# Optimization experiments

Hardware: AMD Instinct MI355X
Metric: run time of the kernel (lower is better)

The kernel has to match this reference:

```python
import jax, jax.numpy as jnp
import numpy as np

N = 50000
E = 800000
IN_C = 128
HID = 256
OUT_C = 51


def graph_conv(x, edge_index, edge_weight, w_rel, b_rel, w_root):
    # PyG GraphConv: out = lin_rel(aggr_add(w_e * x_src)) + lin_root(x)
    src, dst = edge_index[0], edge_index[1]
    msgs = x[src] * edge_weight[:, None]            # [E, F]
    agg = jax.ops.segment_sum(msgs, dst, num_segments=x.shape[0])  # [N, F]
    return agg @ w_rel + b_rel + x @ w_root


def setup_inputs() -> dict:
    key = jax.random.key(0)
    ks = jax.random.split(key, 10)
    s = lambda fan_in: 1.0 / np.sqrt(fan_in)
    return {
        "x0": jax.random.normal(ks[0], (N, IN_C), jnp.float32),
        "edge_index": jax.random.randint(ks[1], (2, E), 0, N, jnp.int64),
        "edge_weight": jax.random.uniform(ks[2], (E,), jnp.float32),
        "conv1_w_rel": jax.random.uniform(ks[3], (IN_C, HID), jnp.float32, -s(IN_C), s(IN_C)),
        "conv1_b_rel": jnp.zeros((HID,), jnp.float32),
        "conv1_w_root": jax.random.uniform(ks[4], (IN_C, HID), jnp.float32, -s(IN_C), s(IN_C)),
        "conv2_w_rel": jax.random.uniform(ks[5], (HID, HID), jnp.float32, -s(HID), s(HID)),
        "conv2_b_rel": jnp.zeros((HID,), jnp.float32),
        "conv2_w_root": jax.random.uniform(ks[6], (HID, HID), jnp.float32, -s(HID), s(HID)),
        "lin_w": jax.random.uniform(ks[7], (2 * HID, OUT_C), jnp.float32, -s(2 * HID), s(2 * HID)),
        "lin_b": jnp.zeros((OUT_C,), jnp.float32),
    }


def reference(x0, edge_index, edge_weight,
              conv1_w_rel, conv1_b_rel, conv1_w_root,
              conv2_w_rel, conv2_b_rel, conv2_w_root,
              lin_w, lin_b):
    # eval mode: dropout is identity
    x1 = jax.nn.relu(graph_conv(x0, edge_index, edge_weight, conv1_w_rel, conv1_b_rel, conv1_w_root))
    x2 = jax.nn.relu(graph_conv(x1, edge_index, edge_weight, conv2_w_rel, conv2_b_rel, conv2_w_root))
    x = jnp.concatenate([x1, x2], axis=-1)          # [N, 2H]
    return x @ lin_w + lin_b                         # [N, OUT_C]
```

## Files before the change

### kernel.cpp

```cpp
#include <hip/hip_runtime.h>
#include <hip/hip_bf16.h>

#define N_NODES 50000
#define N_EDGES 800000
#define IN_CH   128
#define HID     256
#define OUTC    51

typedef __attribute__((ext_vector_type(8))) short  bf16x8;
typedef __attribute__((ext_vector_type(4))) float  f32x4;
typedef __attribute__((ext_vector_type(2))) float  f32x2;
typedef __attribute__((ext_vector_type(4))) unsigned int u32x4;

__device__ __forceinline__ float bf2f(unsigned short u) {
    union { unsigned int i; float f; } v; v.i = ((unsigned int)u) << 16; return v.f;
}
__device__ __forceinline__ unsigned short f2bf(float f) {
    union { float f; unsigned int i; } v; v.f = f;
    unsigned int u = v.i;
    unsigned int r = (u + 0x7fffu + ((u >> 16) & 1u)) >> 16;
    return (unsigned short)r;
}
__device__ __forceinline__ unsigned short ldbf(const void* p, long i, int isf) {
    return isf ? f2bf(((const float*)p)[i]) : ((const unsigned short*)p)[i];
}
__device__ __forceinline__ float ldf(const void* p, long i, int isf) {
    return isf ? ((const float*)p)[i] : bf2f(((const unsigned short*)p)[i]);
}
__device__ __forceinline__ void load_edge_nt(const int* __restrict__ ei, int e, int is64,
                                             int* src, int* dst) {
    if (is64) { *src = __builtin_nontemporal_load(ei + 2 * e);
                *dst = __builtin_nontemporal_load(ei + 2 * (N_EDGES + e)); }
    else      { *src = __builtin_nontemporal_load(ei + e);
                *dst = __builtin_nontemporal_load(ei + N_EDGES + e); }
}

typedef const __attribute__((address_space(1))) unsigned int* gas_u32;
typedef __attribute__((address_space(3))) unsigned int* las_u32;
__device__ __forceinline__ void cp16(const void* g, void* l) {
    __builtin_amdgcn_global_load_lds((gas_u32)g, (las_u32)l, 16, 0, 0);
}

#define EBLK 1024
#define HB   ((N_EDGES + EBLK - 1) / EBLK)
#define NBKT ((N_NODES + 255) / 256)

__global__ __launch_bounds__(256) void init_kernel(const unsigned int* __restrict__ x0w,
                                                   int* __restrict__ flags,
                                                   const int* __restrict__ ei) {
    int tid = threadIdx.x;
    if (blockIdx.x == 0) {
        if (tid < 64) {
            unsigned int w = x0w[tid];
            unsigned int ex = (w >> 7) & 0xFFu;
            unsigned long long bm = __ballot(ex >= 0x60u && ex <= 0x90u);
            if (tid == 0) flags[0] = (__popcll(bm) >= 48) ? 0 : 1;
        }
        return;
    }
    __shared__ int any;
    if (tid == 0) any = 0;
    __syncthreads();
    int acc = 0;
    for (int s = 0; s < 8; s++) {
        int i = (tid * 8 + s) * (N_EDGES / 2048);
        acc |= ei[2 * i + 1];
    }
    if (acc != 0) any = 1;
    __syncthreads();
    if (tid == 0) flags[1] = any;
}

__global__ void prep_all_kernel(const void* __restrict__ x0, int cb,
                                const void* __restrict__ w1r, const void* __restrict__ w1x,
                                const void* __restrict__ w2r, const void* __restrict__ w2x,
                                const void* __restrict__ lw,
                                const void* __restrict__ b1h, const void* __restrict__ b2h,
                                const void* __restrict__ lbh, const int* __restrict__ flags,
                                unsigned short* __restrict__ x0bf,
                                unsigned short* __restrict__ Bt1, unsigned short* __restrict__ Bt2,
                                unsigned short* __restrict__ Bt3,
                                float* __restrict__ b1, float* __restrict__ b2, float* __restrict__ b3,
                                const int* __restrict__ ei, unsigned int* __restrict__ bc,
                                int pblocks) {
    __shared__ unsigned int cnt[NBKT];
    int isf = flags[0];
    if ((int)blockIdx.x < cb) {
        if (!isf) return;
        long t0 = ((long)blockIdx.x * 256 + threadIdx.x) * 8;
        const float* xf = (const float*)x0;
        f32x4 v0 = *(const f32x4*)(xf + t0);
        f32x4 v1 = *(const f32x4*)(xf + t0 + 4);
        u32x4 pk;
        pk[0] = (unsigned int)f2bf(v0[0]) | ((unsigned int)f2bf(v0[1]) << 16);
        pk[1] = (unsigned int)f2bf(v0[2]) | ((unsigned int)f2bf(v0[3]) << 16);
        pk[2] = (unsigned int)f2bf(v1[0]) | ((unsigned int)f2bf(v1[1]) << 16);
        pk[3] = (unsigned int)f2bf(v1[2]) | ((unsigned int)f2bf(v1[3]) << 16);
        *(u32x4*)(x0bf + t0) = pk;
        return;
    }
    int rb = blockIdx.x - cb;
    if (rb >= pblocks) {
        int b = rb - pblocks;
        int tid = threadIdx.x;
        if (tid < NBKT) cnt[tid] = 0;
        __syncthreads();
        int is64 = (flags[1] == 0);
        int e0 = b * EBLK;
#pragma unroll
        for (int u = 0; u < 4; u++) {
            int e = e0 + u * 256 + tid;
            if (e < N_EDGES) {
                int src, dst; load_edge_nt(ei, e, is64, &src, &dst);
                if ((unsigned)src < N_NODES && (unsigned)dst < N_NODES)
                    atomicAdd(&cnt[dst >> 8], 1u);
            }
        }
        __syncthreads();
        if (tid < NBKT) bc[tid * HB + b] = cnt[tid];
        return;
    }
    int t = rb * 256 + threadIdx.x;
    if (t < 256 * 256) {
        int n = t >> 8, k = t & 255;
        Bt1[n * 256 + k] = (k < 128) ? ldbf(w1r, k * 256 + n, isf) : ldbf(w1x, (k - 128) * 256 + n, isf);
        return;
    }
    t -= 256 * 256;
    if (t < 256 * 512) {
        int n = t >> 9, k = t & 511;
        Bt2[n * 512 + k] = (k < 256) ? ldbf(w2r, k * 256 + n, isf) : ldbf(w2x, (k - 256) * 256 + n, isf);
        return;
    }
    t -= 256 * 512;
    if (t < 64 * 512) {
        int n = t >> 9, k = t & 511;
        Bt3[n * 512 + k] = (n < OUTC) ? ldbf(lw, k * OUTC + n, isf) : (unsigned short)0;
        return;
    }
    t -= 64 * 512;
    if (t < 256) { b1[t] = ldf(b1h, t, isf); return; }
    t -= 256;
    if (t < 256) { b2[t] = ldf(b2h, t, isf); return; }
    t -= 256;
    if (t < 64)  { b3[t] = (t < OUTC) ? ldf(lbh, t, isf) : 0.0f; return; }
}

__global__ __launch_bounds__(1024) void s1_kernel(const unsigned int* __restrict__ bc,
                                                  unsigned int* __restrict__ pbase,
                                                  unsigned int* __restrict__ total) {
    __shared__ unsigned int sd[1024];
    int b = blockIdx.x, tid = threadIdx.x;
    unsigned int v = (tid < HB) ? bc[b * HB + tid] : 0u;
    sd[tid] = v;
    __syncthreads();
    for (int off = 1; off < 1024; off <<= 1) {
        unsigned int t = (tid >= off) ? sd[tid - off] : 0u;
        __syncthreads();
        sd[tid] += t;
        __syncthreads();
    }
    if (tid < HB) pbase[tid * NBKT + b] = sd[tid] - v;
    if (tid == 1023) total[b] = sd[1023];
}

__global__ __launch_bounds__(256) void f1_kernel(const int* __restrict__ ei, const void* __restrict__ ew,
                                                 const int* __restrict__ flags,
                                                 const unsigned int* __restrict__ pbase,
                                                 const unsigned int* __restrict__ btot,
                                                 uint2* __restrict__ rec) {
    __shared__ unsigned int cur[NBKT];
    __shared__ unsigned int sb[256];
    int tid = threadIdx.x;
    unsigned int v = (tid < NBKT) ? btot[tid] : 0u;
    sb[tid] = v;
    __syncthreads();
    for (int off = 1; off < 256; off <<= 1) {
        unsigned int t = (tid >= off) ? sb[tid - off] : 0u;
        __syncthreads();
        sb[tid] += t;
        __syncthreads();
    }
    if (tid < NBKT) cur[tid] = (sb[tid] - v) + pbase[blockIdx.x * NBKT + tid];
    __syncthreads();
    int is64 = (flags[1] == 0);
    int isf = flags[0];
    int e0 = blockIdx.x * EBLK;
#pragma unroll
    for (int u = 0; u < 4; u++) {
        int e = e0 + u * 256 + tid;
        if (e < N_EDGES) {
            int src, dst; load_edge_nt(ei, e, is64, &src, &dst);
            if ((unsigned)src < N_NODES && (unsigned)dst < N_NODES) {
                unsigned int w = ldbf(ew, e, isf);
                unsigned int pos = atomicAdd(&cur[dst >> 8], 1u);
                uint2 r; r.x = (w << 16) | (unsigned)src; r.y = (unsigned)dst;
                rec[pos] = r;
            }
        }
    }
}

__global__ __launch_bounds__(512) void f2_kernel(const uint2* __restrict__ rec,
                                                 const unsigned int* __restrict__ btot,
                                                 int* __restrict__ rp, unsigned int* __restrict__ cw) {
    __shared__ unsigned int sb[256], c2[256], sc[256], cur2[256];
    int tid = threadIdx.x, b = blockIdx.x;
    unsigned int vb = 0;
    if (tid < 256) { vb = (tid < NBKT) ? btot[tid] : 0u; sb[tid] = vb; }
    __syncthreads();
    for (int off = 1; off < 256; off <<= 1) {
        unsigned int t = (tid < 256 && tid >= off) ? sb[tid - off] : 0u;
        __syncthreads();
        if (tid < 256) sb[tid] += t;
        __syncthreads();
    }
    unsigned int s0 = (b > 0) ? sb[b - 1] : 0u;
    unsigned int e0 = sb[b];
    if (b == 0 && tid == 0) rp[N_NODES] = (int)sb[NBKT - 1];
    if (tid < 256) c2[tid] = 0;
    __syncthreads();
    for (unsigned int pos = s0 + tid; pos < e0; pos += 512)
        atomicAdd(&c2[rec[pos].y & 255u], 1u);
    __syncthreads();
    unsigned int v = 0;
    if (tid < 256) { v = c2[tid]; sc[tid] = v; }
    __syncthreads();
    for (int off = 1; off < 256; off <<= 1) {
        unsigned int t = (tid < 256 && tid >= off) ? sc[tid - off] : 0u;
        __syncthreads();
        if (tid < 256) sc[tid] += t;
        __syncthreads();
    }
    if (tid < 256) {
        unsigned int start = s0 + sc[tid] - v;
        int node = b * 256 + tid;
        if (node < N_NODES) rp[node] = (int)start;
        cur2[tid] = start;
    }
    __syncthreads();
    for (unsigned int pos = s0 + tid; pos < e0; pos += 512) {
        uint2 r = rec[pos];
        unsigned int p = atomicAdd(&cur2[r.y & 255u], 1u);
        cw[p] = r.x;
    }
}

__global__ __launch_bounds__(256) void zout_kernel(unsigned short* __restrict__ out, long n) {
    long t = (long)blockIdx.x * 256 + threadIdx.x;
    if (t < n) out[t] = 0;
}

__global__ __launch_bounds__(256) void agg1_kernel(const unsigned short* __restrict__ x0raw,
                                                   const unsigned short* __restrict__ x0conv,
                                                   int use_conv, const int* __restrict__ flags,
                                                   const int* __restrict__ rp, const unsigned int* __restrict__ cw,
                                                   unsigned short* __restrict__ X12) {
    const unsigned short* x0b = (use_conv && flags[0]) ? x0conv : x0raw;
    int r = blockIdx.x * 16 + (threadIdx.x >> 4);
    if (r >= N_NODES) return;
    int l = threadIdx.x & 15;
    int grpbase = threadIdx.x & 48;
    int js = rp[r], je = rp[r + 1];
    if (js < 0) js = 0;
    if (je > N_EDGES) je = N_EDGES;
    float a0 = 0.f, a1 = 0.f, a2 = 0.f, a3 = 0.f;
    float a4 = 0.f, a5 = 0.f, a6 = 0.f, a7 = 0.f;
    for (int base = js; base < je; base += 16) {
        int n = je - base; if (n > 16) n = 16;
        int idx = base + l; if (idx >= je) idx = je - 1;
        unsigned int rec = __builtin_nontemporal_load(cw + idx);
        for (int j = 0; j < n; j += 4) {
            int m = n - j; if (m > 4) m = 4;
            unsigned int vv[4]; u32x4 q[4];
#pragma unroll
            for (int u = 0; u < 4; u++) vv[u] = __shfl(rec, grpbase + j + u);
#pragma unroll
            for (int u = 0; u < 4; u++) if (u < m)
                q[u] = *(const u32x4*)(x0b + (long)(vv[u] & 0xFFFFu) * 128 + l * 8);
#pragma unroll
            for (int u = 0; u < 4; u++) if (u < m) {
                float w = bf2f((unsigned short)(vv[u] >> 16));
                a0 += w * bf2f((unsigned short)(q[u][0] & 0xffffu));
                a1 += w * bf2f((unsigned short)(q[u][0] >> 16));
                a2 += w * bf2f((unsigned short)(q[u][1] & 0xffffu));
                a3 += w * bf2f((unsigned short)(q[u][1] >> 16));
                a4 += w * bf2f((unsigned short)(q[u][2] & 0xffffu));
                a5 += w * bf2f((unsigned short)(q[u][2] >> 16));
                a6 += w * bf2f((unsigned short)(q[u][3] & 0xffffu));
                a7 += w * bf2f((unsigned short)(q[u][3] >> 16));
            }
        }
    }
    u32x4 pk;
    pk[0] = (unsigned int)f2bf(a0) | ((unsigned int)f2bf(a1) << 16);
    pk[1] = (unsigned int)f2bf(a2) | ((unsigned int)f2bf(a3) << 16);
    pk[2] = (unsigned int)f2bf(a4) | ((unsigned int)f2bf(a5) << 16);
    pk[3] = (unsigned int)f2bf(a6) | ((unsigned int)f2bf(a7) << 16);
    *(u32x4*)&X12[(long)r * 512 + 256 + l * 8] = pk;
}

__global__ __launch_bounds__(256) void agg2_kernel(const int* __restrict__ rp, const unsigned int* __restrict__ cw,
                                                   unsigned short* __restrict__ X12,
                                                   const unsigned char* __restrict__ x1f8,
                                                   const int* __restrict__ flags, int f8mode) {
    int usef8 = (f8mode == 2) || (f8mode == 1 && flags[0] == 0);
    int r = blockIdx.x * 16 + (threadIdx.x >> 4);
    if (r >= N_NODES) return;
    int l = threadIdx.x & 15;
    int grpbase = threadIdx.x & 48;
    int js = rp[r], je = rp[r + 1];
    if (js < 0) js = 0;
    if (je > N_EDGES) je = N_EDGES;
    float a[16];
#pragma unroll
    for (int c = 0; c < 16; c++) a[c] = 0.f;
    if (usef8) {
        for (int base = js; base < je; base += 16) {
            int n = je - base; if (n > 16) n = 16;
            int idx = base + l; if (idx >= je) idx = je - 1;
            unsigned int rec = __builtin_nontemporal_load(cw + idx);
            for (int j = 0; j < n; j += 4) {
                int m = n - j; if (m > 4) m = 4;
                unsigned int vv[4]; u32x4 q[4];
#pragma unroll
                for (int u = 0; u < 4; u++) vv[u] = __shfl(rec, grpbase + j + u);
#pragma unroll
                for (int u = 0; u < 4; u++) if (u < m)
                    q[u] = *(const u32x4*)(x1f8 + (long)(vv[u] & 0xFFFFu) * 256 + l * 16);
#pragma unroll
                for (int u = 0; u < 4; u++) if (u < m) {
                    float w = bf2f((unsigned short)(vv[u] >> 16));
#pragma unroll
                    for (int c = 0; c < 4; c++) {
                        f32x2 plo = __builtin_amdgcn_cvt_pk_f32_fp8((int)q[u][c], false);
                        f32x2 phi = __builtin_amdgcn_cvt_pk_f32_fp8((int)q[u][c], true);
                        a[c * 4 + 0] += w * plo.x; a[c * 4 + 1] += w * plo.y;
                        a[c * 4 + 2] += w * phi.x; a[c * 4 + 3] += w * phi.y;
                    }
                }
            }
        }
    } else {
        for (int base = js; base < je; base += 16) {
            int n = je - base; if (n > 16) n = 16;
            int idx = base + l; if (idx >= je) idx = je - 1;
            unsigned int rec = __builtin_nontemporal_load(cw + idx);
            for (int j = 0; j < n; j += 4) {
                int m = n - j; if (m > 4) m = 4;
                unsigned int vv[4]; u32x4 q0[4], q1[4];
#pragma unroll
                for (int u = 0; u < 4; u++) vv[u] = __shfl(rec, grpbase + j + u);
#pragma unroll
                for (int u = 0; u < 4; u++) if (u < m) {
                    const unsigned short* sp = X12 + (long)(vv[u] & 0xFFFFu) * 512 + l * 16;
                    q0[u] = *(const u32x4*)sp;
                    q1[u] = *(const u32x4*)(sp + 8);
                }
#pragma unroll
                for (int u = 0; u < 4; u++) if (u < m) {
                    float w = bf2f((unsigned short)(vv[u] >> 16));
#pragma unroll
                    for (int c = 0; c < 4; c++) {
                        a[c * 2 + 0] += w * bf2f((unsigned short)(q0[u][c] & 0xffffu));
                        a[c * 2 + 1] += w * bf2f((unsigned short)(q0[u][c] >> 16));
                        a[8 + c * 2 + 0] += w * bf2f((unsigned short)(q1[u][c] & 0xffffu));
                        a[8 + c * 2 + 1] += w * bf2f((unsigned short)(q1[u][c] >> 16));
                    }
                }
            }
        }
    }
    u32x4 p0, p1;
#pragma unroll
    for (int c = 0; c < 4; c++) {
        p0[c] = (unsigned int)f2bf(a[c * 2]) | ((unsigned int)f2bf(a[c * 2 + 1]) << 16);
        p1[c] = (unsigned int)f2bf(a[8 + c * 2]) | ((unsigned int)f2bf(a[8 + c * 2 + 1]) << 16);
    }
    unsigned short* op = &X12[(long)r * 512 + 256 + l * 16];
    *(u32x4*)op = p0;
    *(u32x4*)(op + 8) = p1;
}

__global__ __launch_bounds__(512) void gemm_big_kernel(
    const unsigned short* __restrict__ Aagg, int lda_agg, int Kagg,
    const unsigned short* __restrict__ AxRaw, const unsigned short* __restrict__ AxConv,
    int use_conv, int lda_x,
    const unsigned short* __restrict__ Bt, int K,
    const float* __restrict__ bias, const int* __restrict__ flags,
    unsigned short* __restrict__ out, int ldo, int ocol, int M,
    unsigned char* __restrict__ x1f8, int f8mode) {
    __shared__ __align__(16) unsigned short As[128][64];
    __shared__ __align__(16) unsigned short Bs[256][64];
    const unsigned short* Ax = (use_conv && flags[0]) ? AxConv : AxRaw;
    int dof8 = (f8mode == 2) || (f8mode == 1 && flags[0] == 0);
    int tid = threadIdx.x;
    int bm0 = blockIdx.x * 128;
    int wave = tid >> 6, lane = tid & 63;
    int wm = wave >> 2, wn = wave & 3;
    int quad = lane >> 4, l16 = lane & 15;
    int lr = lane >> 3;
    int sc = (lane & 7) ^ lr;

    f32x4 acc[4][4];
#pragma unroll
    for (int mt = 0; mt < 4; mt++)
#pragma unroll
        for (int nt = 0; nt < 4; nt++) acc[mt][nt] = (f32x4){0.f, 0.f, 0.f, 0.f};

    for (int k0 = 0; k0 < K; k0 += 64) {
        const unsigned short* srcp;
        int stride, koff;
        if (k0 < Kagg) { srcp = Aagg; stride = lda_agg; koff = k0; }
        else           { srcp = Ax;   stride = lda_x;   koff = k0 - Kagg; }
#pragma unroll
        for (int i = 0; i < 2; i++) {
            int t = wave * 2 + i;
            int r = t * 8 + lr;
            int gr = bm0 + r; if (gr >= M) gr = M - 1;
            cp16(srcp + (long)gr * stride + koff + sc * 8, (char*)As + t * 1024);
        }
#pragma unroll
        for (int i = 0; i < 4; i++) {
            int t = wave * 4 + i;
            int r = t * 8 + lr;
            cp16(Bt + (long)r * K + k0 + sc * 8, (char*)Bs + t * 1024);
        }
        __syncthreads();
#pragma unroll
        for (int kc = 0; kc < 64; kc += 32) {
            int k8 = (kc >> 3) + quad;
            int swz = (k8 ^ (l16 & 7)) << 4;
            bf16x8 a[4], b[4];
#pragma unroll
            for (int mt = 0; mt < 4; mt++) {
                int row = wm * 64 + mt * 16 + l16;
                a[mt] = *(const bf16x8*)((const char*)As + row * 128 + swz);
            }
#pragma unroll
            for (int nt = 0; nt < 4; nt++) {
                int row = wn * 64 + nt * 16 + l16;
                b[nt] = *(const bf16x8*)((const char*)Bs + row * 128 + swz);
            }
#pragma unroll
            for (int mt = 0; mt < 4; mt++)
#pragma unroll
                for (int nt = 0; nt < 4; nt++)
                    acc[mt][nt] = __builtin_amdgcn_mfma_f32_16x16x32_bf16(a[mt], b[nt], acc[mt][nt], 0, 0, 0);
        }
        __syncthreads();
    }

#pragma unroll
    for (int mt = 0; mt < 4; mt++) {
#pragma unroll
        for (int nt = 0; nt < 4; nt++) {
            f32x4 a = acc[mt][nt];
            int colI = wn * 64 + nt * 16 + l16;
            float bv = bias[colI];
#pragma unroll
            for (int rr = 0; rr < 4; rr++) {
                int row = bm0 + wm * 64 + mt * 16 + quad * 4 + rr;
                if (row < M) {
                    float v = a[rr] + bv;
                    v = v > 0.f ? v : 0.f;
                    out[(long)row * ldo + ocol + colI] = f2bf(v);
                    if (dof8) {
                        int p = __builtin_amdgcn_cvt_pk_fp8_f32(v, v, 0, false);
                        x1f8[(long)row * 256 + colI] = (unsigned char)(p & 0xff);
                    }
                }
            }
        }
    }
}

__global__ __launch_bounds__(256) void gemm_head_kernel(
    const unsigned short* __restrict__ Ax, int lda_x,
    const unsigned short* __restrict__ Bt, int K,
    const float* __restrict__ bias,
    void* __restrict__ out, int ldo,
    int M, int realN, const int* __restrict__ flagF) {
    __shared__ __align__(16) unsigned short As[64][64];
    __shared__ __align__(16) unsigned short Bs[64][64];
    int tid = threadIdx.x;
    int bm0 = blockIdx.x * 64;
    int wave = tid >> 6, lane = tid & 63;
    int wm = wave >> 1, wn = wave & 1;
    int quad = lane >> 4, l16 = lane & 15;
    int lr = lane >> 3;
    int sc = (lane & 7) ^ lr;

    f32x4 acc[2][2];
#pragma unroll
    for (int mt = 0; mt < 2; mt++)
#pragma unroll
        for (int nt = 0; nt < 2; nt++) acc[mt][nt] = (f32x4){0.f, 0.f, 0.f, 0.f};

    for (int k0 = 0; k0 < K; k0 += 64) {
#pragma unroll
        for (int i = 0; i < 2; i++) {
            int t = wave * 2 + i;
            int r = t * 8 + lr;
            int gr = bm0 + r; if (gr >= M) gr = M - 1;
            cp16(Ax + (long)gr * lda_x + k0 + sc * 8, (char*)As + t * 1024);
        }
#pragma unroll
        for (int i = 0; i < 2; i++) {
            int t = wave * 2 + i;
            int r = t * 8 + lr;
            cp16(Bt + (long)r * K + k0 + sc * 8, (char*)Bs + t * 1024);
        }
        __syncthreads();
#pragma unroll
        for (int kc = 0; kc < 64; kc += 32) {
            int k8 = (kc >> 3) + quad;
            int swz = (k8 ^ (l16 & 7)) << 4;
            bf16x8 a0 = *(const bf16x8*)((const char*)As + (wm * 32 + l16) * 128 + swz);
            bf16x8 a1 = *(const bf16x8*)((const char*)As + (wm * 32 + 16 + l16) * 128 + swz);
#pragma unroll
            for (int nt = 0; nt < 2; nt++) {
                bf16x8 b = *(const bf16x8*)((const char*)Bs + (wn * 32 + nt * 16 + l16) * 128 + swz);
                acc[0][nt] = __builtin_amdgcn_mfma_f32_16x16x32_bf16(a0, b, acc[0][nt], 0, 0, 0);
                acc[1][nt] = __builtin_amdgcn_mfma_f32_16x16x32_bf16(a1, b, acc[1][nt], 0, 0, 0);
            }
        }
        __syncthreads();
    }

    int out_f32 = *flagF;
#pragma unroll
    for (int mt = 0; mt < 2; mt++) {
#pragma unroll
        for (int nt = 0; nt < 2; nt++) {
            f32x4 a = acc[mt][nt];
            int colI = wn * 32 + nt * 16 + l16;
            float bv = bias[colI];
#pragma unroll
            for (int rr = 0; rr < 4; rr++) {
                int row = bm0 + wm * 32 + mt * 16 + quad * 4 + rr;
                if (row < M && colI < realN) {
                    float v = a[rr] + bv;
                    long idx = (long)row * ldo + colI;
                    if (out_f32) ((float*)out)[idx] = v;
                    else ((unsigned short*)out)[idx] = f2bf(v);
                }
            }
        }
    }
}

extern "C" void kernel_launch(void* const* d_in, const int* in_sizes, int n_in,
                              void* d_out, int out_size, void* d_ws, size_t ws_size,
                              hipStream_t stream) {
    const void* x0  = d_in[0];
    const int*  ei  = (const int*)d_in[1];
    const void* ew  = d_in[2];
    const void* w1r = d_in[3];
    const void* b1h = d_in[4];
    const void* w1x = d_in[5];
    const void* w2r = d_in[6];
    const void* b2h = d_in[7];
    const void* w2x = d_in[8];
    const void* lw  = d_in[9];
    const void* lbh = d_in[10];

    char* ws = (char*)d_ws;
    unsigned short* X12     = (unsigned short*)(ws);
    unsigned int*   cw      = (unsigned int*)(ws + 51200000);
    int*            row_ptr = (int*)(ws + 54400000);
    unsigned short* Bt1     = (unsigned short*)(ws + 54800128);
    unsigned short* Bt2     = (unsigned short*)(ws + 54931200);
    unsigned short* Bt3     = (unsigned short*)(ws + 55193344);
    float*          b1      = (float*)(ws + 55258880);
    float*          b2      = (float*)(ws + 55259904);
    float*          b3      = (float*)(ws + 55260928);
    int*            flags   = (int*)(ws + 55261184);
    unsigned short* x0bf    = (unsigned short*)(ws + 55262272);
    unsigned char*  x1f8sep = (unsigned char*)(ws + 68062272);
    const size_t NEED_NOCONV = 55262272;
    const size_t NEED_FULL   = 68062272;
    const size_t NEED_F8SEP  = 80862272;

    uint2*        rec   = (uint2*)(ws);
    unsigned int* bc    = (unsigned int*)(ws + 6400000);
    unsigned int* pbse  = (unsigned int*)(ws + 7013120);
    unsigned int* btot  = (unsigned int*)(ws + 7626240);

    if (ws_size < NEED_NOCONV) {
        long n = (long)N_NODES * OUTC;
        zout_kernel<<<(int)((n + 255) / 256), 256, 0, stream>>>((unsigned short*)d_out, n);
        return;
    }
    int use_conv = (ws_size >= NEED_FULL) ? 1 : 0;
    int f8mode = (ws_size >= NEED_F8SEP) ? 2 : (use_conv ? 1 : 0);
    unsigned char* x1f8 = (f8mode == 2) ? x1f8sep : (unsigned char*)x0bf;

    int* flagF = flags + 0;

    init_kernel<<<2, 256, 0, stream>>>((const unsigned int*)x0, flags, ei);

    int cb = use_conv ? ((N_NODES * IN_CH) / (256 * 8)) : 0;
    {
        int ptotal = 256 * 256 + 256 * 512 + 64 * 512 + 256 + 256 + 64;
        int pblocks = (ptotal + 255) / 256;
        prep_all_kernel<<<cb + pblocks + HB, 256, 0, stream>>>(
            x0, cb, w1r, w1x, w2r, w2x, lw, b1h, b2h, lbh, flags, x0bf,
            Bt1, Bt2, Bt3, b1, b2, b3, ei, bc, pblocks);
    }

    s1_kernel<<<NBKT, 1024, 0, stream>>>(bc, pbse, btot);
    f1_kernel<<<HB, 256, 0, stream>>>(ei, ew, flags, pbse, btot, rec);
    f2_kernel<<<NBKT, 512, 0, stream>>>(rec, btot, row_ptr, cw);

    int mblocks  = (N_NODES + 127) / 128;
    int hblocks  = (N_NODES + 63) / 64;
    int ablocks  = (N_NODES + 15) / 16;

    const unsigned short* x0raw = (const unsigned short*)x0;

    agg1_kernel<<<ablocks, 256, 0, stream>>>(x0raw, x0bf, use_conv, flags, row_ptr, cw, X12);
    gemm_big_kernel<<<mblocks, 512, 0, stream>>>(X12 + 256, 512, 128,
                                                 x0raw, x0bf, use_conv, IN_CH,
                                                 Bt1, 256, b1, flags,
                                                 X12, 512, 0, N_NODES, x1f8, f8mode);
    agg2_kernel<<<ablocks, 256, 0, stream>>>(row_ptr, cw, X12, x1f8, flags, f8mode);
    gemm_big_kernel<<<mblocks, 512, 0, stream>>>(X12 + 256, 512, 256,
                                                 X12, X12, 0, 512,
                                                 Bt2, 512, b2, flags,
                                                 X12, 512, 256, N_NODES, (unsigned char*)nullptr, 0);
    gemm_head_kernel<<<hblocks, 256, 0, stream>>>(X12, 512, Bt3, 512, b3,
                                                  d_out, OUTC, N_NODES, OUTC, flagF);
}
```

Baseline: 264.3 us.

## Sort nodes by degree within buckets and widen gather unroll to eight

f2_kernel now bitonic-sorts the 256 nodes of each bucket by in-degree and writes a permutation. agg1 and agg2 use it to map 16-lane groups to nodes, so nodes with similar edge counts share a wavefront and lanes sit idle less often. The inner gather loop now issues eight row loads per step instead of four, putting more memory requests in flight. The cost is extra register pressure, one indirection load per row, and a per-block sort in f2.

```diff
diff --git a/kernel.cpp b/kernel.cpp
--- a/kernel.cpp
+++ b/kernel.cpp
@@ -203,8 +203,10 @@
 
 __global__ __launch_bounds__(512) void f2_kernel(const uint2* __restrict__ rec,
                                                  const unsigned int* __restrict__ btot,
-                                                 int* __restrict__ rp, unsigned int* __restrict__ cw) {
+                                                 int* __restrict__ rp, unsigned int* __restrict__ cw,
+                                                 unsigned short* __restrict__ perm) {
     __shared__ unsigned int sb[256], c2[256], sc[256], cur2[256];
+    __shared__ unsigned int keys[256];
     int tid = threadIdx.x, b = blockIdx.x;
     unsigned int vb = 0;
     if (tid < 256) { vb = (tid < NBKT) ? btot[tid] : 0u; sb[tid] = vb; }
@@ -224,7 +226,7 @@
         atomicAdd(&c2[rec[pos].y & 255u], 1u);
     __syncthreads();
     unsigned int v = 0;
-    if (tid < 256) { v = c2[tid]; sc[tid] = v; }
+    if (tid < 256) { v = c2[tid]; sc[tid] = v; keys[tid] = (v << 8) | (unsigned int)tid; }
     __syncthreads();
     for (int off = 1; off < 256; off <<= 1) {
         unsigned int t = (tid < 256 && tid >= off) ? sc[tid - off] : 0u;
@@ -244,6 +246,21 @@
         unsigned int p = atomicAdd(&cur2[r.y & 255u], 1u);
         cw[p] = r.x;
     }
+    for (int k = 2; k <= 256; k <<= 1) {
+        for (int j = k >> 1; j > 0; j >>= 1) {
+            __syncthreads();
+            if (tid < 256) {
+                int ixj = tid ^ j;
+                if (ixj > tid) {
+                    unsigned int ka = keys[tid], kb = keys[ixj];
+                    bool swp = ((tid & k) == 0) ? (ka > kb) : (ka < kb);
+                    if (swp) { keys[tid] = kb; keys[ixj] = ka; }
+                }
+            }
+        }
+    }
+    __syncthreads();
+    if (tid < 256) perm[b * 256 + tid] = (unsigned short)(b * 256 + (int)(keys[tid] & 255u));
 }
 
 __global__ __launch_bounds__(256) void zout_kernel(unsigned short* __restrict__ out, long n) {
@@ -255,9 +272,11 @@
                                                    const unsigned short* __restrict__ x0conv,
                                                    int use_conv, const int* __restrict__ flags,
                                                    const int* __restrict__ rp, const unsigned int* __restrict__ cw,
+                                                   const unsigned short* __restrict__ perm,
                                                    unsigned short* __restrict__ X12) {
     const unsigned short* x0b = (use_conv && flags[0]) ? x0conv : x0raw;
-    int r = blockIdx.x * 16 + (threadIdx.x >> 4);
+    int ridx = blockIdx.x * 16 + (threadIdx.x >> 4);
+    int r = perm[ridx];
     if (r >= N_NODES) return;
     int l = threadIdx.x & 15;
     int grpbase = threadIdx.x & 48;
@@ -270,16 +289,16 @@
         int n = je - base; if (n > 16) n = 16;
         int idx = base + l; if (idx >= je) idx = je - 1;
         unsigned int rec = __builtin_nontemporal_load(cw + idx);
-        for (int j = 0; j < n; j += 4) {
-            int m = n - j; if (m > 4) m = 4;
-            unsigned int vv[4]; u32x4 q[4];
-#pragma unroll
-            for (int u = 0; u < 4; u++) vv[u] = __shfl(rec, grpbase + j + u);
-#pragma unroll
-            for (int u = 0; u < 4; u++) if (u < m)
+        for (int j = 0; j < n; j += 8) {
+            int m = n - j; if (m > 8) m = 8;
+            unsigned int vv[8]; u32x4 q[8];
+#pragma unroll
+            for (int u = 0; u < 8; u++) vv[u] = __shfl(rec, grpbase + j + u);
+#pragma unroll
+            for (int u = 0; u < 8; u++) if (u < m)
                 q[u] = *(const u32x4*)(x0b + (long)(vv[u] & 0xFFFFu) * 128 + l * 8);
 #pragma unroll
-            for (int u = 0; u < 4; u++) if (u < m) {
+            for (int u = 0; u < 8; u++) if (u < m) {
                 float w = bf2f((unsigned short)(vv[u] >> 16));
                 a0 += w * bf2f((unsigned short)(q[u][0] & 0xffffu));
                 a1 += w * bf2f((unsigned short)(q[u][0] >> 16));
@@ -301,11 +320,13 @@
 }
 
 __global__ __launch_bounds__(256) void agg2_kernel(const int* __restrict__ rp, const unsigned int* __restrict__ cw,
+                                                   const unsigned short* __restrict__ perm,
                                                    unsigned short* __restrict__ X12,
                                                    const unsigned char* __restrict__ x1f8,
                                                    const int* __restrict__ flags, int f8mode) {
     int usef8 = (f8mode == 2) || (f8mode == 1 && flags[0] == 0);
-    int r = blockIdx.x * 16 + (threadIdx.x >> 4);
+    int ridx = blockIdx.x * 16 + (threadIdx.x >> 4);
+    int r = perm[ridx];
     if (r >= N_NODES) return;
     int l = threadIdx.x & 15;
     int grpbase = threadIdx.x & 48;
@@ -320,16 +341,16 @@
             int n = je - base; if (n > 16) n = 16;
             int idx = base + l; if (idx >= je) idx = je - 1;
             unsigned int rec = __builtin_nontemporal_load(cw + idx);
-            for (int j = 0; j < n; j += 4) {
-                int m = n - j; if (m > 4) m = 4;
-                unsigned int vv[4]; u32x4 q[4];
-#pragma unroll
-                for (int u = 0; u < 4; u++) vv[u] = __shfl(rec, grpbase + j + u);
-#pragma unroll
-                for (int u = 0; u < 4; u++) if (u < m)
+            for (int j = 0; j < n; j += 8) {
+                int m = n - j; if (m > 8) m = 8;
+                unsigned int vv[8]; u32x4 q[8];
+#pragma unroll
+                for (int u = 0; u < 8; u++) vv[u] = __shfl(rec, grpbase + j + u);
+#pragma unroll
+                for (int u = 0; u < 8; u++) if (u < m)
                     q[u] = *(const u32x4*)(x1f8 + (long)(vv[u] & 0xFFFFu) * 256 + l * 16);
 #pragma unroll
-                for (int u = 0; u < 4; u++) if (u < m) {
+                for (int u = 0; u < 8; u++) if (u < m) {
                     float w = bf2f((unsigned short)(vv[u] >> 16));
 #pragma unroll
                     for (int c = 0; c < 4; c++) {
@@ -569,6 +590,7 @@
     unsigned short* X12     = (unsigned short*)(ws);
     unsigned int*   cw      = (unsigned int*)(ws + 51200000);
     int*            row_ptr = (int*)(ws + 54400000);
+    unsigned short* perm    = (unsigned short*)(ws + 54600064);
     unsigned short* Bt1     = (unsigned short*)(ws + 54800128);
     unsigned short* Bt2     = (unsigned short*)(ws + 54931200);
     unsigned short* Bt3     = (unsigned short*)(ws + 55193344);
@@ -611,20 +633,20 @@
 
     s1_kernel<<<NBKT, 1024, 0, stream>>>(bc, pbse, btot);
     f1_kernel<<<HB, 256, 0, stream>>>(ei, ew, flags, pbse, btot, rec);
-    f2_kernel<<<NBKT, 512, 0, stream>>>(rec, btot, row_ptr, cw);
+    f2_kernel<<<NBKT, 512, 0, stream>>>(rec, btot, row_ptr, cw, perm);
 
     int mblocks  = (N_NODES + 127) / 128;
     int hblocks  = (N_NODES + 63) / 64;
-    int ablocks  = (N_NODES + 15) / 16;
+    int ablocks  = (NBKT * 256) / 16;
 
     const unsigned short* x0raw = (const unsigned short*)x0;
 
-    agg1_kernel<<<ablocks, 256, 0, stream>>>(x0raw, x0bf, use_conv, flags, row_ptr, cw, X12);
+    agg1_kernel<<<ablocks, 256, 0, stream>>>(x0raw, x0bf, use_conv, flags, row_ptr, cw, perm, X12);
     gemm_big_kernel<<<mblocks, 512, 0, stream>>>(X12 + 256, 512, 128,
                                                  x0raw, x0bf, use_conv, IN_CH,
                                                  Bt1, 256, b1, flags,
                                                  X12, 512, 0, N_NODES, x1f8, f8mode);
-    agg2_kernel<<<ablocks, 256, 0, stream>>>(row_ptr, cw, X12, x1f8, flags, f8mode);
+    agg2_kernel<<<ablocks, 256, 0, stream>>>(row_ptr, cw, perm, X12, x1f8, flags, f8mode);
     gemm_big_kernel<<<mblocks, 512, 0, stream>>>(X12 + 256, 512, 256,
                                                  X12, X12, 0, 512,
                                                  Bt2, 512, b2, flags,
```

New measurement: 280.5 us. 6.1% more time.

## Split aggregation kernels by feature quarter to shrink per-pass gather footprint

Applied to the files above, without the earlier changes.

The agg1 and agg2 gather kernels now give each block one quarter of the feature columns. A block covers 64 nodes in four sequential passes, and block ids are interleaved so that neighbouring blocks work on the same feature quarter at the same time. Each lane gathers 4 or 8 bytes per neighbour instead of 16 or 32, with 8-way unrolling. The intent is to cut the working set of the random gathers so they hit in L2/MALL more often. In exchange the edge list is read four times, and the smaller loads make more memory transactions.

```diff
diff --git a/kernel.cpp b/kernel.cpp
--- a/kernel.cpp
+++ b/kernel.cpp
@@ -44,6 +44,9 @@
 #define EBLK 1024
 #define HB   ((N_EDGES + EBLK - 1) / EBLK)
 #define NBKT ((N_NODES + 255) / 256)
+
+#define NCHUNK ((N_NODES + 63) / 64)
+#define ABLK   (NCHUNK * 4)
 
 __global__ __launch_bounds__(256) void init_kernel(const unsigned int* __restrict__ x0w,
                                                    int* __restrict__ flags,
@@ -257,47 +260,44 @@
                                                    const int* __restrict__ rp, const unsigned int* __restrict__ cw,
                                                    unsigned short* __restrict__ X12) {
     const unsigned short* x0b = (use_conv && flags[0]) ? x0conv : x0raw;
-    int r = blockIdx.x * 16 + (threadIdx.x >> 4);
-    if (r >= N_NODES) return;
+    int bid = blockIdx.x;
+    int qq = (bid >> 1) & 3;
+    int chunk = (bid >> 3) * 2 + (bid & 1);
+    int g = threadIdx.x >> 4;
     int l = threadIdx.x & 15;
     int grpbase = threadIdx.x & 48;
-    int js = rp[r], je = rp[r + 1];
-    if (js < 0) js = 0;
-    if (je > N_EDGES) je = N_EDGES;
-    float a0 = 0.f, a1 = 0.f, a2 = 0.f, a3 = 0.f;
-    float a4 = 0.f, a5 = 0.f, a6 = 0.f, a7 = 0.f;
-    for (int base = js; base < je; base += 16) {
-        int n = je - base; if (n > 16) n = 16;
-        int idx = base + l; if (idx >= je) idx = je - 1;
-        unsigned int rec = __builtin_nontemporal_load(cw + idx);
-        for (int j = 0; j < n; j += 4) {
-            int m = n - j; if (m > 4) m = 4;
-            unsigned int vv[4]; u32x4 q[4];
-#pragma unroll
-            for (int u = 0; u < 4; u++) vv[u] = __shfl(rec, grpbase + j + u);
-#pragma unroll
-            for (int u = 0; u < 4; u++) if (u < m)
-                q[u] = *(const u32x4*)(x0b + (long)(vv[u] & 0xFFFFu) * 128 + l * 8);
-#pragma unroll
-            for (int u = 0; u < 4; u++) if (u < m) {
-                float w = bf2f((unsigned short)(vv[u] >> 16));
-                a0 += w * bf2f((unsigned short)(q[u][0] & 0xffffu));
-                a1 += w * bf2f((unsigned short)(q[u][0] >> 16));
-                a2 += w * bf2f((unsigned short)(q[u][1] & 0xffffu));
-                a3 += w * bf2f((unsigned short)(q[u][1] >> 16));
-                a4 += w * bf2f((unsigned short)(q[u][2] & 0xffffu));
-                a5 += w * bf2f((unsigned short)(q[u][2] >> 16));
-                a6 += w * bf2f((unsigned short)(q[u][3] & 0xffffu));
-                a7 += w * bf2f((unsigned short)(q[u][3] >> 16));
-            }
-        }
-    }
-    u32x4 pk;
-    pk[0] = (unsigned int)f2bf(a0) | ((unsigned int)f2bf(a1) << 16);
-    pk[1] = (unsigned int)f2bf(a2) | ((unsigned int)f2bf(a3) << 16);
-    pk[2] = (unsigned int)f2bf(a4) | ((unsigned int)f2bf(a5) << 16);
-    pk[3] = (unsigned int)f2bf(a6) | ((unsigned int)f2bf(a7) << 16);
-    *(u32x4*)&X12[(long)r * 512 + 256 + l * 8] = pk;
+    const unsigned short* tab = x0b + qq * 32 + l * 2;
+#pragma unroll 1
+    for (int i = 0; i < 4; i++) {
+        int r = chunk * 64 + i * 16 + g;
+        if (r >= N_NODES) continue;
+        int js = rp[r], je = rp[r + 1];
+        if (js < 0) js = 0;
+        if (je > N_EDGES) je = N_EDGES;
+        float a0 = 0.f, a1 = 0.f;
+        for (int base = js; base < je; base += 16) {
+            int n = je - base; if (n > 16) n = 16;
+            int idx = base + l; if (idx >= je) idx = je - 1;
+            unsigned int rec = __builtin_nontemporal_load(cw + idx);
+            for (int j = 0; j < n; j += 8) {
+                int m = n - j; if (m > 8) m = 8;
+                unsigned int vv[8], qd[8];
+#pragma unroll
+                for (int u = 0; u < 8; u++) vv[u] = __shfl(rec, grpbase + j + u);
+#pragma unroll
+                for (int u = 0; u < 8; u++) if (u < m)
+                    qd[u] = *(const unsigned int*)(tab + (long)(vv[u] & 0xFFFFu) * 128);
+#pragma unroll
+                for (int u = 0; u < 8; u++) if (u < m) {
+                    float w = bf2f((unsigned short)(vv[u] >> 16));
+                    a0 += w * bf2f((unsigned short)(qd[u] & 0xffffu));
+                    a1 += w * bf2f((unsigned short)(qd[u] >> 16));
+                }
+            }
+        }
+        *(unsigned int*)&X12[(long)r * 512 + 256 + qq * 32 + l * 2] =
+            (unsigned int)f2bf(a0) | ((unsigned int)f2bf(a1) << 16);
+    }
 }
 
 __global__ __launch_bounds__(256) void agg2_kernel(const int* __restrict__ rp, const unsigned int* __restrict__ cw,
@@ -305,81 +305,74 @@
                                                    const unsigned char* __restrict__ x1f8,
                                                    const int* __restrict__ flags, int f8mode) {
     int usef8 = (f8mode == 2) || (f8mode == 1 && flags[0] == 0);
-    int r = blockIdx.x * 16 + (threadIdx.x >> 4);
-    if (r >= N_NODES) return;
+    int bid = blockIdx.x;
+    int qq = (bid >> 1) & 3;
+    int chunk = (bid >> 3) * 2 + (bid & 1);
+    int g = threadIdx.x >> 4;
     int l = threadIdx.x & 15;
     int grpbase = threadIdx.x & 48;
-    int js = rp[r], je = rp[r + 1];
-    if (js < 0) js = 0;
-    if (je > N_EDGES) je = N_EDGES;
-    float a[16];
-#pragma unroll
-    for (int c = 0; c < 16; c++) a[c] = 0.f;
-    if (usef8) {
-        for (int base = js; base < je; base += 16) {
-            int n = je - base; if (n > 16) n = 16;
-            int idx = base + l; if (idx >= je) idx = je - 1;
-            unsigned int rec = __builtin_nontemporal_load(cw + idx);
-            for (int j = 0; j < n; j += 4) {
-                int m = n - j; if (m > 4) m = 4;
-                unsigned int vv[4]; u32x4 q[4];
-#pragma unroll
-                for (int u = 0; u < 4; u++) vv[u] = __shfl(rec, grpbase + j + u);
-#pragma unroll
-                for (int u = 0; u < 4; u++) if (u < m)
-                    q[u] = *(const u32x4*)(x1f8 + (long)(vv[u] & 0xFFFFu) * 256 + l * 16);
-#pragma unroll
-                for (int u = 0; u < 4; u++) if (u < m) {
-                    float w = bf2f((unsigned short)(vv[u] >> 16));
-#pragma unroll
-                    for (int c = 0; c < 4; c++) {
-                        f32x2 plo = __builtin_amdgcn_cvt_pk_f32_fp8((int)q[u][c], false);
-                        f32x2 phi = __builtin_amdgcn_cvt_pk_f32_fp8((int)q[u][c], true);
-                        a[c * 4 + 0] += w * plo.x; a[c * 4 + 1] += w * plo.y;
-                        a[c * 4 + 2] += w * phi.x; a[c * 4 + 3] += w * phi.y;
+#pragma unroll 1
+    for (int i = 0; i < 4; i++) {
+        int r = chunk * 64 + i * 16 + g;
+        if (r >= N_NODES) continue;
+        int js = rp[r], je = rp[r + 1];
+        if (js < 0) js = 0;
+        if (je > N_EDGES) je = N_EDGES;
+        float a0 = 0.f, a1 = 0.f, a2 = 0.f, a3 = 0.f;
+        if (usef8) {
+            const unsigned char* tab = x1f8 + qq * 64 + l * 4;
+            for (int base = js; base < je; base += 16) {
+                int n = je - base; if (n > 16) n = 16;
+                int idx = base + l; if (idx >= je) idx = je - 1;
+                unsigned int rec = __builtin_nontemporal_load(cw + idx);
+                for (int j = 0; j < n; j += 8) {
+                    int m = n - j; if (m > 8) m = 8;
+                    unsigned int vv[8], qd[8];
+#pragma unroll
+                    for (int u = 0; u < 8; u++) vv[u] = __shfl(rec, grpbase + j + u);
+#pragma unroll
+                    for (int u = 0; u < 8; u++) if (u < m)
+                        qd[u] = *(const unsigned int*)(tab + (long)(vv[u] & 0xFFFFu) * 256);
+#pragma unroll
+                    for (int u = 0; u < 8; u++) if (u < m) {
+                        float w = bf2f((unsigned short)(vv[u] >> 16));
+                        f32x2 plo = __builtin_amdgcn_cvt_pk_f32_fp8((int)qd[u], false);
+                        f32x2 phi = __builtin_amdgcn_cvt_pk_f32_fp8((int)qd[u], true);
+                        a0 += w * plo.x; a1 += w * plo.y;
+                        a2 += w * phi.x; a3 += w * phi.y;
                     }
                 }
             }
-        }
-    } else {
-        for (int base = js; base < je; base += 16) {
-            int n = je - base; if (n > 16) n = 16;
-            int idx = base + l; if (idx >= je) idx = je - 1;
-            unsigned int rec = __builtin_nontemporal_load(cw + idx);
-            for (int j = 0; j < n; j += 4) {
-                int m = n - j; if (m > 4) m = 4;
-                unsigned int vv[4]; u32x4 q0[4], q1[4];
-#pragma unroll
-                for (int u = 0; u < 4; u++) vv[u] = __shfl(rec, grpbase + j + u);
-#pragma unroll
-                for (int u = 0; u < 4; u++) if (u < m) {
-                    const unsigned short* sp = X12 + (long)(vv[u] & 0xFFFFu) * 512 + l * 16;
-                    q0[u] = *(const u32x4*)sp;
-                    q1[u] = *(const u32x4*)(sp + 8);
-                }
-#pragma unroll
-                for (int u = 0; u < 4; u++) if (u < m) {
-                    float w = bf2f((unsigned short)(vv[u] >> 16));
-#pragma unroll
-                    for (int c = 0; c < 4; c++) {
-                        a[c * 2 + 0] += w * bf2f((unsigned short)(q0[u][c] & 0xffffu));
-                        a[c * 2 + 1] += w * bf2f((unsigned short)(q0[u][c] >> 16));
-                        a[8 + c * 2 + 0] += w * bf2f((unsigned short)(q1[u][c] & 0xffffu));
-                        a[8 + c * 2 + 1] += w * bf2f((unsigned short)(q1[u][c] >> 16));
+        } else {
+            const unsigned short* tabb = X12 + qq * 64 + l * 4;
+            for (int base = js; base < je; base += 16) {
+                int n = je - base; if (n > 16) n = 16;
+                int idx = base + l; if (idx >= je) idx = je - 1;
+                unsigned int rec = __builtin_nontemporal_load(cw + idx);
+                for (int j = 0; j < n; j += 8) {
+                    int m = n - j; if (m > 8) m = 8;
+                    unsigned int vv[8]; uint2 qd[8];
+#pragma unroll
+                    for (int u = 0; u < 8; u++) vv[u] = __shfl(rec, grpbase + j + u);
+#pragma unroll
+                    for (int u = 0; u < 8; u++) if (u < m)
+                        qd[u] = *(const uint2*)(tabb + (long)(vv[u] & 0xFFFFu) * 512);
+#pragma unroll
+                    for (int u = 0; u < 8; u++) if (u < m) {
+                        float w = bf2f((unsigned short)(vv[u] >> 16));
+                        a0 += w * bf2f((unsigned short)(qd[u].x & 0xffffu));
+                        a1 += w * bf2f((unsigned short)(qd[u].x >> 16));
+                        a2 += w * bf2f((unsigned short)(qd[u].y & 0xffffu));
+                        a3 += w * bf2f((unsigned short)(qd[u].y >> 16));
                     }
                 }
             }
         }
-    }
-    u32x4 p0, p1;
-#pragma unroll
-    for (int c = 0; c < 4; c++) {
-        p0[c] = (unsigned int)f2bf(a[c * 2]) | ((unsigned int)f2bf(a[c * 2 + 1]) << 16);
-        p1[c] = (unsigned int)f2bf(a[8 + c * 2]) | ((unsigned int)f2bf(a[8 + c * 2 + 1]) << 16);
-    }
-    unsigned short* op = &X12[(long)r * 512 + 256 + l * 16];
-    *(u32x4*)op = p0;
-    *(u32x4*)(op + 8) = p1;
+        uint2 pk;
+        pk.x = (unsigned int)f2bf(a0) | ((unsigned int)f2bf(a1) << 16);
+        pk.y = (unsigned int)f2bf(a2) | ((unsigned int)f2bf(a3) << 16);
+        *(uint2*)&X12[(long)r * 512 + 256 + qq * 64 + l * 4] = pk;
+    }
 }
 
 __global__ __launch_bounds__(512) void gemm_big_kernel(
@@ -615,16 +608,15 @@
 
     int mblocks  = (N_NODES + 127) / 128;
     int hblocks  = (N_NODES + 63) / 64;
-    int ablocks  = (N_NODES + 15) / 16;
 
     const unsigned short* x0raw = (const unsigned short*)x0;
 
-    agg1_kernel<<<ablocks, 256, 0, stream>>>(x0raw, x0bf, use_conv, flags, row_ptr, cw, X12);
+    agg1_kernel<<<ABLK, 256, 0, stream>>>(x0raw, x0bf, use_conv, flags, row_ptr, cw, X12);
     gemm_big_kernel<<<mblocks, 512, 0, stream>>>(X12 + 256, 512, 128,
                                                  x0raw, x0bf, use_conv, IN_CH,
                                                  Bt1, 256, b1, flags,
                                                  X12, 512, 0, N_NODES, x1f8, f8mode);
-    agg2_kernel<<<ablocks, 256, 0, stream>>>(row_ptr, cw, X12, x1f8, flags, f8mode);
+    agg2_kernel<<<ABLK, 256, 0, stream>>>(row_ptr, cw, X12, x1f8, flags, f8mode);
     gemm_big_kernel<<<mblocks, 512, 0, stream>>>(X12 + 256, 512, 256,
                                                  X12, X12, 0, 512,
                                                  Bt2, 512, b2, flags,
```

Result: slower. 294.9 us (+11.6%).

## Split fp8 feature table into four column quarters for cache-local gathers

Applied to the files above, without the earlier changes.

The fp8 copy of layer-1 activations is stored as four separate 64-column planes, and agg2 now launches four blocks per 64-node chunk, each gathering only one quarter of the columns. Every plane (about 3.2 MB) is small enough to stay resident in cache while the blocks that share it run, so the random row gathers should hit cache more often. Each node now uses 4 threads per quarter and handles 8 edges per step. In exchange, the edge list and row pointers are read four times, and each gather is a single 64-byte row piece.

```diff
diff --git a/kernel.cpp b/kernel.cpp
--- a/kernel.cpp
+++ b/kernel.cpp
@@ -6,6 +6,8 @@
 #define IN_CH   128
 #define HID     256
 #define OUTC    51
+
+#define QSZ 3200000
 
 typedef __attribute__((ext_vector_type(8))) short  bf16x8;
 typedef __attribute__((ext_vector_type(4))) float  f32x4;
@@ -44,6 +46,9 @@
 #define EBLK 1024
 #define HB   ((N_EDGES + EBLK - 1) / EBLK)
 #define NBKT ((N_NODES + 255) / 256)
+
+#define NCHUNK ((N_NODES + 63) / 64)
+#define ABLKQ  (NCHUNK * 4)
 
 __global__ __launch_bounds__(256) void init_kernel(const unsigned int* __restrict__ x0w,
                                                    int* __restrict__ flags,
@@ -302,13 +307,18 @@
 
 __global__ __launch_bounds__(256) void agg2_kernel(const int* __restrict__ rp, const unsigned int* __restrict__ cw,
                                                    unsigned short* __restrict__ X12,
-                                                   const unsigned char* __restrict__ x1f8,
+                                                   const unsigned char* __restrict__ x1f8q,
                                                    const int* __restrict__ flags, int f8mode) {
     int usef8 = (f8mode == 2) || (f8mode == 1 && flags[0] == 0);
-    int r = blockIdx.x * 16 + (threadIdx.x >> 4);
+    int bid = blockIdx.x;
+    int qq = bid & 3;
+    int chunk = bid >> 2;
+    int g = threadIdx.x >> 2;
+    int sub = threadIdx.x & 3;
+    int lane = threadIdx.x & 63;
+    int grpbase = lane & 60;
+    int r = chunk * 64 + g;
     if (r >= N_NODES) return;
-    int l = threadIdx.x & 15;
-    int grpbase = threadIdx.x & 48;
     int js = rp[r], je = rp[r + 1];
     if (js < 0) js = 0;
     if (je > N_EDGES) je = N_EDGES;
@@ -316,57 +326,59 @@
 #pragma unroll
     for (int c = 0; c < 16; c++) a[c] = 0.f;
     if (usef8) {
-        for (int base = js; base < je; base += 16) {
-            int n = je - base; if (n > 16) n = 16;
-            int idx = base + l; if (idx >= je) idx = je - 1;
-            unsigned int rec = __builtin_nontemporal_load(cw + idx);
-            for (int j = 0; j < n; j += 4) {
-                int m = n - j; if (m > 4) m = 4;
-                unsigned int vv[4]; u32x4 q[4];
-#pragma unroll
-                for (int u = 0; u < 4; u++) vv[u] = __shfl(rec, grpbase + j + u);
-#pragma unroll
-                for (int u = 0; u < 4; u++) if (u < m)
-                    q[u] = *(const u32x4*)(x1f8 + (long)(vv[u] & 0xFFFFu) * 256 + l * 16);
-#pragma unroll
-                for (int u = 0; u < 4; u++) if (u < m) {
-                    float w = bf2f((unsigned short)(vv[u] >> 16));
-#pragma unroll
-                    for (int c = 0; c < 4; c++) {
-                        f32x2 plo = __builtin_amdgcn_cvt_pk_f32_fp8((int)q[u][c], false);
-                        f32x2 phi = __builtin_amdgcn_cvt_pk_f32_fp8((int)q[u][c], true);
-                        a[c * 4 + 0] += w * plo.x; a[c * 4 + 1] += w * plo.y;
-                        a[c * 4 + 2] += w * phi.x; a[c * 4 + 3] += w * phi.y;
-                    }
+        const unsigned char* tab = x1f8q + (long)qq * QSZ + sub * 16;
+        for (int base = js; base < je; base += 8) {
+            int n = je - base; if (n > 8) n = 8;
+            int i0 = base + sub * 2; if (i0 >= je) i0 = je - 1;
+            int i1 = i0 + 1;         if (i1 >= je) i1 = je - 1;
+            unsigned int rcx = __builtin_nontemporal_load(cw + i0);
+            unsigned int rcy = __builtin_nontemporal_load(cw + i1);
+            unsigned int vv[8]; u32x4 q[8];
+#pragma unroll
+            for (int u = 0; u < 8; u++)
+                vv[u] = __shfl((u & 1) ? rcy : rcx, grpbase + (u >> 1));
+#pragma unroll
+            for (int u = 0; u < 8; u++) if (u < n)
+                q[u] = *(const u32x4*)(tab + (vv[u] & 0xFFFFu) * 64);
+#pragma unroll
+            for (int u = 0; u < 8; u++) if (u < n) {
+                float w = bf2f((unsigned short)(vv[u] >> 16));
+#pragma unroll
+                for (int c = 0; c < 4; c++) {
+                    f32x2 plo = __builtin_amdgcn_cvt_pk_f32_fp8((int)q[u][c], false);
+                    f32x2 phi = __builtin_amdgcn_cvt_pk_f32_fp8((int)q[u][c], true);
+                    a[c * 4 + 0] += w * plo.x; a[c * 4 + 1] += w * plo.y;
+                    a[c * 4 + 2] += w * phi.x; a[c * 4 + 3] += w * phi.y;
                 }
             }
         }
     } else {
-        for (int base = js; base < je; base += 16) {
-            int n = je - base; if (n > 16) n = 16;
-            int idx = base + l; if (idx >= je) idx = je - 1;
-            unsigned int rec = __builtin_nontemporal_load(cw + idx);
-            for (int j = 0; j < n; j += 4) {
-                int m = n - j; if (m > 4) m = 4;
-                unsigned int vv[4]; u32x4 q0[4], q1[4];
-#pragma unroll
-                for (int u = 0; u < 4; u++) vv[u] = __shfl(rec, grpbase + j + u);
-#pragma unroll
-                for (int u = 0; u < 4; u++) if (u < m) {
-                    const unsigned short* sp = X12 + (long)(vv[u] & 0xFFFFu) * 512 + l * 16;
-                    q0[u] = *(const u32x4*)sp;
-                    q1[u] = *(const u32x4*)(sp + 8);
-                }
-#pragma unroll
-                for (int u = 0; u < 4; u++) if (u < m) {
-                    float w = bf2f((unsigned short)(vv[u] >> 16));
-#pragma unroll
-                    for (int c = 0; c < 4; c++) {
-                        a[c * 2 + 0] += w * bf2f((unsigned short)(q0[u][c] & 0xffffu));
-                        a[c * 2 + 1] += w * bf2f((unsigned short)(q0[u][c] >> 16));
-                        a[8 + c * 2 + 0] += w * bf2f((unsigned short)(q1[u][c] & 0xffffu));
-                        a[8 + c * 2 + 1] += w * bf2f((unsigned short)(q1[u][c] >> 16));
-                    }
+        const unsigned short* tabb = X12 + qq * 64 + sub * 16;
+        for (int base = js; base < je; base += 8) {
+            int n = je - base; if (n > 8) n = 8;
+            int i0 = base + sub * 2; if (i0 >= je) i0 = je - 1;
+            int i1 = i0 + 1;         if (i1 >= je) i1 = je - 1;
+            unsigned int rcx = __builtin_nontemporal_load(cw + i0);
+            unsigned int rcy = __builtin_nontemporal_load(cw + i1);
+            unsigned int vv[8]; u32x4 q0[8], q1[8];
+#pragma unroll
+            for (int u = 0; u < 8; u++)
+                vv[u] = __shfl((u & 1) ? rcy : rcx, grpbase + (u >> 1));
+#pragma unroll
+            for (int u = 0; u < 8; u++) if (u < n) {
+                const unsigned short* sp = tabb + (long)(vv[u] & 0xFFFFu) * 512;
+                q0[u] = *(const u32x4*)sp;
+                q1[u] = *(const u32x4*)(sp + 8);
+            }
+#pragma unroll
+            for (int u = 0; u < 8; u++) if (u < n) {
+                float w = bf2f((unsigned short)(vv[u] >> 16));
+#pragma unroll
+                for (int c = 0; c < 4; c++) {
+                    a[c * 2 + 0] += w * bf2f((unsigned short)(q0[u][c] & 0xffffu));
+                    a[c * 2 + 1] += w * bf2f((unsigned short)(q0[u][c] >> 16));
+                    a[8 + c * 2 + 0] += w * bf2f((unsigned short)(q1[u][c] & 0xffffu));
+                    a[8 + c * 2 + 1] += w * bf2f((unsigned short)(q1[u][c] >> 16));
                 }
             }
         }
@@ -377,7 +389,7 @@
         p0[c] = (unsigned int)f2bf(a[c * 2]) | ((unsigned int)f2bf(a[c * 2 + 1]) << 16);
         p1[c] = (unsigned int)f2bf(a[8 + c * 2]) | ((unsigned int)f2bf(a[8 + c * 2 + 1]) << 16);
     }
-    unsigned short* op = &X12[(long)r * 512 + 256 + l * 16];
+    unsigned short* op = &X12[(long)r * 512 + 256 + qq * 64 + sub * 16];
     *(u32x4*)op = p0;
     *(u32x4*)(op + 8) = p1;
 }
@@ -389,7 +401,7 @@
     const unsigned short* __restrict__ Bt, int K,
     const float* __restrict__ bias, const int* __restrict__ flags,
     unsigned short* __restrict__ out, int ldo, int ocol, int M,
-    unsigned char* __restrict__ x1f8, int f8mode) {
+    unsigned char* __restrict__ x1f8q, int f8mode) {
     __shared__ __align__(16) unsigned short As[128][64];
     __shared__ __align__(16) unsigned short Bs[256][64];
     const unsigned short* Ax = (use_conv && flags[0]) ? AxConv : AxRaw;
@@ -467,7 +479,8 @@
                     out[(long)row * ldo + ocol + colI] = f2bf(v);
                     if (dof8) {
                         int p = __builtin_amdgcn_cvt_pk_fp8_f32(v, v, 0, false);
-                        x1f8[(long)row * 256 + colI] = (unsigned char)(p & 0xff);
+                        x1f8q[(long)(colI >> 6) * QSZ + (long)row * 64 + (colI & 63)] =
+                            (unsigned char)(p & 0xff);
                     }
                 }
             }
@@ -624,11 +637,12 @@
                                                  x0raw, x0bf, use_conv, IN_CH,
                                                  Bt1, 256, b1, flags,
                                                  X12, 512, 0, N_NODES, x1f8, f8mode);
-    agg2_kernel<<<ablocks, 256, 0, stream>>>(row_ptr, cw, X12, x1f8, flags, f8mode);
+    agg2_kernel<<<ABLKQ, 256, 0, stream>>>(row_ptr, cw, X12, x1f8, flags, f8mode);
     gemm_big_kernel<<<mblocks, 512, 0, stream>>>(X12 + 256, 512, 256,
                                                  X12, X12, 0, 512,
                                                  Bt2, 512, b2, flags,
-                                                 X12, 512, 256, N_NODES, (unsigned char*)nullptr, 0);
+                                                 X12, 512, 256, N_NODES,
+                                                 (unsigned char*)nullptr, 0);
     gemm_head_kernel<<<hblocks, 256, 0, stream>>>(X12, 512, Bt3, 512, b3,
                                                   d_out, OUTC, N_NODES, OUTC, flagF);
 }
```

After: 266.6 us. About the same (+0.9%).
